# Performance work log

Measured on AMD Instinct MI355X. Metric: run time of the kernel, lower is better.

Reference implementation:

```python
import jax, jax.numpy as jnp
import numpy as np

DT = 0.01  # module-level constant in the original source
H = 64


def _lstm_cell(x_in, h, c, W_ih, W_hh, b_ih, b_hh):
    # torch nn.LSTM gate order: i, f, g, o
    gates = x_in @ W_ih.T + h @ W_hh.T + (b_ih + b_hh)
    i, f, g, o = jnp.split(gates, 4, axis=-1)
    i = jax.nn.sigmoid(i)
    f = jax.nn.sigmoid(f)
    g = jnp.tanh(g)
    o = jax.nn.sigmoid(o)
    c_new = f * c + i * g
    h_new = o * jnp.tanh(c_new)
    return h_new, c_new


def setup_inputs() -> dict:
    key = jax.random.key(0)
    ks = jax.random.split(key, 12)
    B, x_size, s_size = 4096, 8, 8
    in_size = x_size + s_size
    sc = 1.0 / np.sqrt(H)

    def rn(k, shape, scale=1.0):
        return (jax.random.normal(k, shape, dtype=jnp.float32) * scale)

    return {
        "x": rn(ks[0], (B, 1, x_size)),
        "s0": rn(ks[1], (B, s_size)),
        "W_ih0": rn(ks[2], (4 * H, in_size), sc),
        "W_hh0": rn(ks[3], (4 * H, H), sc),
        "b_ih0": rn(ks[4], (4 * H,), sc),
        "b_hh0": rn(ks[5], (4 * H,), sc),
        "W_ih1": rn(ks[6], (4 * H, H), sc),
        "W_hh1": rn(ks[7], (4 * H, H), sc),
        "b_ih1": rn(ks[8], (4 * H,), sc),
        "b_hh1": rn(ks[9], (4 * H,), sc),
        "fc_W": rn(ks[10], (s_size, H), sc),
        "fc_b": rn(ks[11], (s_size,), sc),
        "num_steps": 1001,  # floor(max_time/dt)+1 with max_time=10.0
    }


def reference(x, s0, W_ih0, W_hh0, b_ih0, b_hh0, W_ih1, W_hh1, b_ih1, b_hh1,
              fc_W, fc_b, num_steps):
    B = x.shape[0]
    xin = x[:, 0, :]  # forward only ever reads x[:, 0:1] -> [B, x_size]
    h0 = jnp.zeros((B, H), x.dtype)

    def step(carry, _):
        s, h_a, c_a, h_b, c_b = carry
        combined = jnp.concatenate([xin, s], axis=-1)  # [B, x_size + s_size]
        h_a, c_a = _lstm_cell(combined, h_a, c_a, W_ih0, W_hh0, b_ih0, b_hh0)
        h_b, c_b = _lstm_cell(h_a, h_b, c_b, W_ih1, W_hh1, b_ih1, b_hh1)
        step_out = h_b @ fc_W.T + fc_b            # [B, s_size]
        s_new = s + step_out * DT                  # Euler integration
        return (s_new, h_a, c_a, h_b, c_b), (s_new, step_out)

    init = (s0, h0, h0, h0, h0)
    _, (outs, res) = jax.lax.scan(step, init, None, length=num_steps)
    outputs = jnp.transpose(outs, (1, 0, 2))       # [B, num_steps, s_size]
    res_step = jnp.transpose(res, (1, 0, 2))       # [B, num_steps, s_size]
    cal_times = jnp.arange(num_steps, dtype=jnp.float32) * DT
    return outputs, cal_times, res_step
```

## Files before the change

kernel.cpp:

```cpp
#include <hip/hip_runtime.h>

#define DTC 0.01f
#define LAM  2.88539008178f
#define L2E  1.44269504089f

typedef __attribute__((ext_vector_type(8))) short short8;
typedef __attribute__((ext_vector_type(4))) float floatx4;

#if __has_builtin(__builtin_amdgcn_exp2f)
#define EXP2F(x) __builtin_amdgcn_exp2f(x)
#else
#define EXP2F(x) exp2f(x)
#endif
#if __has_builtin(__builtin_amdgcn_rcpf)
#define RCPF(x) __builtin_amdgcn_rcpf(x)
#else
#define RCPF(x) (1.0f / (x))
#endif

__device__ __forceinline__ unsigned short f2bf(float f) {
    unsigned u = __float_as_uint(f);
    u += 0x7FFFu + ((u >> 16) & 1u);
    return (unsigned short)(u >> 16);
}
__device__ __forceinline__ float rcp1p(float y) {
    return RCPF(1.0f + EXP2F(y));
}
__device__ __forceinline__ void wg_barrier() {
    asm volatile("s_waitcnt lgkmcnt(0)" ::: "memory");
    __builtin_amdgcn_s_barrier();
}

#define U1S 136

#define MFMA(a, b, c) __builtin_amdgcn_mfma_f32_16x16x32_bf16((a), (b), (c), 0, 0, 0)

__global__ __launch_bounds__(256, 1) void lstm_mfma(
    const float* __restrict__ x,    const float* __restrict__ s0,
    const float* __restrict__ W_ih0,const float* __restrict__ W_hh0,
    const float* __restrict__ b_ih0,const float* __restrict__ b_hh0,
    const float* __restrict__ W_ih1,const float* __restrict__ W_hh1,
    const float* __restrict__ b_ih1,const float* __restrict__ b_hh1,
    const float* __restrict__ fc_W, const float* __restrict__ fc_b,
    const int* __restrict__ nsp,    float* __restrict__ out, int B)
{
    __shared__ __align__(16) unsigned short U1[16 * U1S];

    const int ns   = nsp[0];
    const int tid  = threadIdx.x;
    const int lane = tid & 63;
    const int wave = tid >> 6;
    const int il   = lane & 15;
    const int quad = lane >> 4;
    const int bb   = blockIdx.x * 16;

    float* cal = out + (size_t)B * ns * 8;
    float* res = cal + ns;

    if (blockIdx.x == 0)
        for (int t = tid; t < ns; t += 256) cal[t] = t * DTC;

    for (int i = tid; i < 16 * U1S; i += 256) U1[i] = 0;

    short8 B0[4][2], B1[4][4], M2f[4][2], BF[2];
    floatx4 gs[4], bias1v[4];
    float gd[4];

    for (int j = 0; j < 4; ++j) {
        const float gam = (j == 2) ? LAM : -L2E;
        const int n = 64 * j + 16 * wave + il;
        float ws[8];
        #pragma unroll
        for (int p = 0; p < 8; ++p) ws[p] = W_ih0[n * 16 + 8 + p];

        #pragma unroll
        for (int kk = 0; kk < 2; ++kk) {
            short8 f;
            #pragma unroll
            for (int jj = 0; jj < 8; ++jj) {
                int k = 32 * kk + 8 * quad + jj;
                f[jj] = (short)f2bf(gam * W_hh0[n * 64 + k]);
            }
            B0[j][kk] = f;
        }
        #pragma unroll
        for (int kk = 0; kk < 4; ++kk) {
            short8 f;
            #pragma unroll
            for (int jj = 0; jj < 8; ++jj) {
                int k = 32 * kk + 8 * quad + jj;
                float w = (k < 64) ? W_ih1[n * 64 + k] : W_hh1[n * 64 + (k - 64)];
                f[jj] = (short)f2bf(gam * w);
            }
            B1[j][kk] = f;
        }
        #pragma unroll
        for (int kk = 0; kk < 2; ++kk) {
            short8 f;
            #pragma unroll
            for (int jj = 0; jj < 8; ++jj) {
                int k = 32 * kk + 8 * quad + jj;
                float acc = 0.0f;
                #pragma unroll
                for (int p = 0; p < 8; ++p) acc += ws[p] * fc_W[p * 64 + k];
                f[jj] = (short)f2bf(gam * DTC * acc);
            }
            M2f[j][kk] = f;
        }
        float accb = 0.0f;
        #pragma unroll
        for (int p = 0; p < 8; ++p) accb += ws[p] * fc_b[p];
        gd[j] = gam * DTC * accb;

        float bcol = b_ih0[n] + b_hh0[n];
        floatx4 gv;
        #pragma unroll
        for (int reg = 0; reg < 4; ++reg) {
            int m = 4 * quad + reg;
            float acc = bcol;
            #pragma unroll
            for (int k = 0; k < 8; ++k) acc += x[(bb + m) * 8 + k] * W_ih0[n * 16 + k];
            #pragma unroll
            for (int p = 0; p < 8; ++p) acc += ws[p] * s0[(bb + m) * 8 + p];
            gv[reg] = gam * acc - gd[j];
        }
        gs[j] = gv;
        float b1 = gam * (b_ih1[n] + b_hh1[n]);
        bias1v[j] = (floatx4){b1, b1, b1, b1};
    }
    #pragma unroll
    for (int kk = 0; kk < 2; ++kk) {
        short8 f;
        #pragma unroll
        for (int jj = 0; jj < 8; ++jj) {
            int k = 32 * kk + 8 * quad + jj;
            float w = (il < 8) ? fc_W[il * 64 + k] : 0.0f;
            f[jj] = (short)f2bf(w);
        }
        BF[kk] = f;
    }
    const float fcb = (il < 8) ? fc_b[il] : 0.0f;

    float cA[4] = {0, 0, 0, 0}, cB[4] = {0, 0, 0, 0};
    float s_reg[4];
    #pragma unroll
    for (int reg = 0; reg < 4; ++reg) {
        int m = 4 * quad + reg;
        s_reg[reg] = (il < 8) ? s0[(bb + m) * 8 + il] : 0.0f;
    }

    short8 a10 = {0, 0, 0, 0, 0, 0, 0, 0};
    short8 a11 = {0, 0, 0, 0, 0, 0, 0, 0};
    const int iidx = 16 * wave + il;
    wg_barrier();

    #pragma unroll 1
    for (int t = 0; t < ns; ++t) {
        short8 a12 = *(const short8*)&U1[il * U1S + 64 + 8 * quad];
        short8 a13 = *(const short8*)&U1[il * U1S + 96 + 8 * quad];

        floatx4 g0[4];
        #pragma unroll
        for (int j = 0; j < 4; ++j) {
            floatx4 z = {0.f, 0.f, 0.f, 0.f};
            z = MFMA(a10, B0[j][0], z);
            z = MFMA(a11, B0[j][1], z);
            g0[j] = z;
        }
        #pragma unroll
        for (int j = 0; j < 4; ++j) {
            floatx4 z = gs[j];
            z = MFMA(a12, M2f[j][0], z);
            z = MFMA(a13, M2f[j][1], z);
            #pragma unroll
            for (int reg = 0; reg < 4; ++reg) z[reg] += gd[j];
            gs[j] = z;
        }
        floatx4 p1[4];
        #pragma unroll
        for (int j = 0; j < 4; ++j) {
            floatx4 z = bias1v[j];
            z = MFMA(a12, B1[j][2], z);
            z = MFMA(a13, B1[j][3], z);
            p1[j] = z;
        }
        #pragma unroll
        for (int reg = 0; reg < 4; ++reg) {
            float iv = rcp1p(g0[0][reg] + gs[0][reg]);
            float fv = rcp1p(g0[1][reg] + gs[1][reg]);
            float gr = rcp1p(g0[2][reg] + gs[2][reg]);
            float gl = __builtin_fmaf(gr, -2.0f * LAM, LAM);
            float ov = rcp1p(g0[3][reg] + gs[3][reg]);
            float c  = __builtin_fmaf(fv, cA[reg], iv * gl);
            cA[reg]  = c;
            float r2 = rcp1p(c);
            float u  = ov * r2;
            float h  = __builtin_fmaf(-2.0f, u, ov);
            U1[(4 * quad + reg) * U1S + iidx] = f2bf(h);
        }
        wg_barrier();

        a10 = *(const short8*)&U1[il * U1S + 0  + 8 * quad];
        a11 = *(const short8*)&U1[il * U1S + 32 + 8 * quad];

        if (t && wave == 0) {
            floatx4 so = {fcb, fcb, fcb, fcb};
            so = MFMA(a12, BF[0], so);
            so = MFMA(a13, BF[1], so);
            #pragma unroll
            for (int reg = 0; reg < 4; ++reg) {
                s_reg[reg] += so[reg] * DTC;
                if (il < 8) {
                    int m = 4 * quad + reg;
                    size_t o = ((size_t)(bb + m) * ns + (t - 1)) * 8 + il;
                    out[o] = s_reg[reg];
                    res[o] = so[reg];
                }
            }
        }

        floatx4 g1[4];
        #pragma unroll
        for (int j = 0; j < 4; ++j) {
            floatx4 z = p1[j];
            z = MFMA(a10, B1[j][0], z);
            z = MFMA(a11, B1[j][1], z);
            g1[j] = z;
        }
        #pragma unroll
        for (int reg = 0; reg < 4; ++reg) {
            float iv = rcp1p(g1[0][reg]);
            float fv = rcp1p(g1[1][reg]);
            float gr = rcp1p(g1[2][reg]);
            float gl = __builtin_fmaf(gr, -2.0f * LAM, LAM);
            float ov = rcp1p(g1[3][reg]);
            float c  = __builtin_fmaf(fv, cB[reg], iv * gl);
            cB[reg]  = c;
            float r2 = rcp1p(c);
            float u  = ov * r2;
            float h  = __builtin_fmaf(-2.0f, u, ov);
            U1[(4 * quad + reg) * U1S + 64 + iidx] = f2bf(h);
        }
        wg_barrier();
    }

    if (wave == 0) {
        short8 a12 = *(const short8*)&U1[il * U1S + 64 + 8 * quad];
        short8 a13 = *(const short8*)&U1[il * U1S + 96 + 8 * quad];
        floatx4 so = {fcb, fcb, fcb, fcb};
        so = MFMA(a12, BF[0], so);
        so = MFMA(a13, BF[1], so);
        #pragma unroll
        for (int reg = 0; reg < 4; ++reg) {
            s_reg[reg] += so[reg] * DTC;
            if (il < 8) {
                int m = 4 * quad + reg;
                size_t o = ((size_t)(bb + m) * ns + (ns - 1)) * 8 + il;
                out[o] = s_reg[reg];
                res[o] = so[reg];
            }
        }
    }
}

extern "C" void kernel_launch(void* const* d_in, const int* in_sizes, int n_in,
                              void* d_out, int out_size, void* d_ws, size_t ws_size,
                              hipStream_t stream) {
    const float* x     = (const float*)d_in[0];
    const float* s0    = (const float*)d_in[1];
    const float* W_ih0 = (const float*)d_in[2];
    const float* W_hh0 = (const float*)d_in[3];
    const float* b_ih0 = (const float*)d_in[4];
    const float* b_hh0 = (const float*)d_in[5];
    const float* W_ih1 = (const float*)d_in[6];
    const float* W_hh1 = (const float*)d_in[7];
    const float* b_ih1 = (const float*)d_in[8];
    const float* b_hh1 = (const float*)d_in[9];
    const float* fc_W  = (const float*)d_in[10];
    const float* fc_b  = (const float*)d_in[11];
    const int*   nsp   = (const int*)d_in[12];
    (void)d_ws; (void)ws_size; (void)n_in; (void)out_size;
    int B = in_sizes[0] / 8;
    dim3 grid(B / 16), block(256);
    hipLaunchKernelGGL(lstm_mfma, grid, block, 0, stream,
        x, s0, W_ih0, W_hh0, b_ih0, b_hh0, W_ih1, W_hh1, b_ih1, b_hh1,
        fc_W, fc_b, nsp, (float*)d_out, B);
}
```

Measured before the change: 1.399 ms.

## Split gate computation across twice the waves with LDS exchange of preactivations

Doubles the workgroup from 4 to 8 waves so each wave computes two of the four gate blocks instead of all four. Gate preactivations are written to a new shared float buffer, and after a barrier each wave reads all four gates for its slice of elements to apply the cell update. This halves the MFMA and activation work per wave per step so more of the serial recurrence runs in parallel. In exchange it adds two extra workgroup barriers and LDS round trips per timestep on a latency-bound loop.

Result: slower. 1.501 ms (+7.2%).

```diff
diff --git a/kernel.cpp b/kernel.cpp
--- a/kernel.cpp
+++ b/kernel.cpp
@@ -32,10 +32,11 @@
 }
 
 #define U1S 136
+#define ES  68
 
 #define MFMA(a, b, c) __builtin_amdgcn_mfma_f32_16x16x32_bf16((a), (b), (c), 0, 0, 0)
 
-__global__ __launch_bounds__(256, 1) void lstm_mfma(
+__global__ __launch_bounds__(512, 1) void lstm_mfma(
     const float* __restrict__ x,    const float* __restrict__ s0,
     const float* __restrict__ W_ih0,const float* __restrict__ W_hh0,
     const float* __restrict__ b_ih0,const float* __restrict__ b_hh0,
@@ -45,6 +46,7 @@
     const int* __restrict__ nsp,    float* __restrict__ out, int B)
 {
     __shared__ __align__(16) unsigned short U1[16 * U1S];
+    __shared__ float E[4 * 16 * ES];
 
     const int ns   = nsp[0];
     const int tid  = threadIdx.x;
@@ -52,26 +54,30 @@
     const int wave = tid >> 6;
     const int il   = lane & 15;
     const int quad = lane >> 4;
+    const int g    = wave >> 1;
+    const int p    = wave & 1;
+    const int col  = 16 * g + il;
     const int bb   = blockIdx.x * 16;
 
     float* cal = out + (size_t)B * ns * 8;
     float* res = cal + ns;
 
     if (blockIdx.x == 0)
-        for (int t = tid; t < ns; t += 256) cal[t] = t * DTC;
-
-    for (int i = tid; i < 16 * U1S; i += 256) U1[i] = 0;
-
-    short8 B0[4][2], B1[4][4], M2f[4][2], BF[2];
-    floatx4 gs[4], bias1v[4];
-    float gd[4];
-
-    for (int j = 0; j < 4; ++j) {
+        for (int t = tid; t < ns; t += 512) cal[t] = t * DTC;
+
+    for (int i = tid; i < 16 * U1S; i += 512) U1[i] = 0;
+
+    short8 B0[2][2], B1[2][4], M2f[2][2], BF[2];
+    floatx4 gs[2];
+    float gd[2], b1s[2];
+
+    for (int jl = 0; jl < 2; ++jl) {
+        const int j = 2 * p + jl;
         const float gam = (j == 2) ? LAM : -L2E;
-        const int n = 64 * j + 16 * wave + il;
+        const int n = 64 * j + col;
         float ws[8];
         #pragma unroll
-        for (int p = 0; p < 8; ++p) ws[p] = W_ih0[n * 16 + 8 + p];
+        for (int pp = 0; pp < 8; ++pp) ws[pp] = W_ih0[n * 16 + 8 + pp];
 
         #pragma unroll
         for (int kk = 0; kk < 2; ++kk) {
@@ -81,7 +87,7 @@
                 int k = 32 * kk + 8 * quad + jj;
                 f[jj] = (short)f2bf(gam * W_hh0[n * 64 + k]);
             }
-            B0[j][kk] = f;
+            B0[jl][kk] = f;
         }
         #pragma unroll
         for (int kk = 0; kk < 4; ++kk) {
@@ -92,7 +98,7 @@
                 float w = (k < 64) ? W_ih1[n * 64 + k] : W_hh1[n * 64 + (k - 64)];
                 f[jj] = (short)f2bf(gam * w);
             }
-            B1[j][kk] = f;
+            B1[jl][kk] = f;
         }
         #pragma unroll
         for (int kk = 0; kk < 2; ++kk) {
@@ -102,15 +108,15 @@
                 int k = 32 * kk + 8 * quad + jj;
                 float acc = 0.0f;
                 #pragma unroll
-                for (int p = 0; p < 8; ++p) acc += ws[p] * fc_W[p * 64 + k];
+                for (int pp = 0; pp < 8; ++pp) acc += ws[pp] * fc_W[pp * 64 + k];
                 f[jj] = (short)f2bf(gam * DTC * acc);
             }
-            M2f[j][kk] = f;
+            M2f[jl][kk] = f;
         }
         float accb = 0.0f;
         #pragma unroll
-        for (int p = 0; p < 8; ++p) accb += ws[p] * fc_b[p];
-        gd[j] = gam * DTC * accb;
+        for (int pp = 0; pp < 8; ++pp) accb += ws[pp] * fc_b[pp];
+        gd[jl] = gam * DTC * accb;
 
         float bcol = b_ih0[n] + b_hh0[n];
         floatx4 gv;
@@ -121,12 +127,11 @@
             #pragma unroll
             for (int k = 0; k < 8; ++k) acc += x[(bb + m) * 8 + k] * W_ih0[n * 16 + k];
             #pragma unroll
-            for (int p = 0; p < 8; ++p) acc += ws[p] * s0[(bb + m) * 8 + p];
-            gv[reg] = gam * acc - gd[j];
-        }
-        gs[j] = gv;
-        float b1 = gam * (b_ih1[n] + b_hh1[n]);
-        bias1v[j] = (floatx4){b1, b1, b1, b1};
+            for (int pp = 0; pp < 8; ++pp) acc += ws[pp] * s0[(bb + m) * 8 + pp];
+            gv[reg] = gam * acc - gd[jl];
+        }
+        gs[jl] = gv;
+        b1s[jl] = gam * (b_ih1[n] + b_hh1[n]);
     }
     #pragma unroll
     for (int kk = 0; kk < 2; ++kk) {
@@ -141,67 +146,70 @@
     }
     const float fcb = (il < 8) ? fc_b[il] : 0.0f;
 
-    float cA[4] = {0, 0, 0, 0}, cB[4] = {0, 0, 0, 0};
+    float cA[2] = {0, 0}, cB[2] = {0, 0};
     float s_reg[4];
     #pragma unroll
-    for (int reg = 0; reg < 4; ++reg) {
-        int m = 4 * quad + reg;
-        s_reg[reg] = (il < 8) ? s0[(bb + m) * 8 + il] : 0.0f;
-    }
-
-    short8 a10 = {0, 0, 0, 0, 0, 0, 0, 0};
-    short8 a11 = {0, 0, 0, 0, 0, 0, 0, 0};
-    const int iidx = 16 * wave + il;
+    for (int reg = 0; reg < 4; ++reg)
+        s_reg[reg] = (il < 8) ? s0[(bb + 4 * quad + reg) * 8 + il] : 0.0f;
+
+    short8 a10 = {0,0,0,0,0,0,0,0};
+    short8 a11 = {0,0,0,0,0,0,0,0};
+    floatx4 p1[2];
+
+    const unsigned short* Ar = &U1[il * U1S + 8 * quad];
+    unsigned short* Hw = &U1[(8 * p + 2 * quad) * U1S + col];
+    float* Ew = &E[(32 * p + 4 * quad) * ES + col];
+    const float* Er = &E[(8 * p + 2 * quad) * ES + col];
+
     wg_barrier();
 
     #pragma unroll 1
     for (int t = 0; t < ns; ++t) {
-        short8 a12 = *(const short8*)&U1[il * U1S + 64 + 8 * quad];
-        short8 a13 = *(const short8*)&U1[il * U1S + 96 + 8 * quad];
-
-        floatx4 g0[4];
-        #pragma unroll
-        for (int j = 0; j < 4; ++j) {
-            floatx4 z = {0.f, 0.f, 0.f, 0.f};
-            z = MFMA(a10, B0[j][0], z);
-            z = MFMA(a11, B0[j][1], z);
-            g0[j] = z;
-        }
-        #pragma unroll
-        for (int j = 0; j < 4; ++j) {
-            floatx4 z = gs[j];
-            z = MFMA(a12, M2f[j][0], z);
-            z = MFMA(a13, M2f[j][1], z);
-            #pragma unroll
-            for (int reg = 0; reg < 4; ++reg) z[reg] += gd[j];
-            gs[j] = z;
-        }
-        floatx4 p1[4];
-        #pragma unroll
-        for (int j = 0; j < 4; ++j) {
-            floatx4 z = bias1v[j];
-            z = MFMA(a12, B1[j][2], z);
-            z = MFMA(a13, B1[j][3], z);
-            p1[j] = z;
-        }
-        #pragma unroll
-        for (int reg = 0; reg < 4; ++reg) {
-            float iv = rcp1p(g0[0][reg] + gs[0][reg]);
-            float fv = rcp1p(g0[1][reg] + gs[1][reg]);
-            float gr = rcp1p(g0[2][reg] + gs[2][reg]);
+        short8 a12 = *(const short8*)(Ar + 64);
+        short8 a13 = *(const short8*)(Ar + 96);
+
+        #pragma unroll
+        for (int jl = 0; jl < 2; ++jl) {
+            floatx4 z = gs[jl];
+            z = MFMA(a12, M2f[jl][0], z);
+            z = MFMA(a13, M2f[jl][1], z);
+            #pragma unroll
+            for (int r = 0; r < 4; ++r) z[r] += gd[jl];
+            gs[jl] = z;
+            floatx4 q = z;
+            q = MFMA(a10, B0[jl][0], q);
+            q = MFMA(a11, B0[jl][1], q);
+            #pragma unroll
+            for (int r = 0; r < 4; ++r)
+                Ew[jl * (16 * ES) + r * ES] = q[r];
+            floatx4 pz = {b1s[jl], b1s[jl], b1s[jl], b1s[jl]};
+            pz = MFMA(a13, B1[jl][3], pz);
+            pz = MFMA(a12, B1[jl][2], pz);
+            p1[jl] = pz;
+        }
+        wg_barrier();
+
+        #pragma unroll
+        for (int e = 0; e < 2; ++e) {
+            float pi = Er[e * ES + 0 * (16 * ES)];
+            float pf = Er[e * ES + 1 * (16 * ES)];
+            float pg = Er[e * ES + 2 * (16 * ES)];
+            float po = Er[e * ES + 3 * (16 * ES)];
+            float iv = rcp1p(pi);
+            float fv = rcp1p(pf);
+            float gr = rcp1p(pg);
+            float ov = rcp1p(po);
             float gl = __builtin_fmaf(gr, -2.0f * LAM, LAM);
-            float ov = rcp1p(g0[3][reg] + gs[3][reg]);
-            float c  = __builtin_fmaf(fv, cA[reg], iv * gl);
-            cA[reg]  = c;
+            float c  = __builtin_fmaf(fv, cA[e], iv * gl);
+            cA[e]    = c;
             float r2 = rcp1p(c);
-            float u  = ov * r2;
-            float h  = __builtin_fmaf(-2.0f, u, ov);
-            U1[(4 * quad + reg) * U1S + iidx] = f2bf(h);
+            float h  = __builtin_fmaf(-2.0f, ov * r2, ov);
+            Hw[e * U1S] = f2bf(h);
         }
         wg_barrier();
 
-        a10 = *(const short8*)&U1[il * U1S + 0  + 8 * quad];
-        a11 = *(const short8*)&U1[il * U1S + 32 + 8 * quad];
+        a10 = *(const short8*)(Ar + 0);
+        a11 = *(const short8*)(Ar + 32);
 
         if (t && wave == 0) {
             floatx4 so = {fcb, fcb, fcb, fcb};
@@ -211,42 +219,47 @@
             for (int reg = 0; reg < 4; ++reg) {
                 s_reg[reg] += so[reg] * DTC;
                 if (il < 8) {
-                    int m = 4 * quad + reg;
-                    size_t o = ((size_t)(bb + m) * ns + (t - 1)) * 8 + il;
+                    size_t o = ((size_t)(bb + 4 * quad + reg) * ns + (t - 1)) * 8 + il;
                     out[o] = s_reg[reg];
                     res[o] = so[reg];
                 }
             }
         }
 
-        floatx4 g1[4];
-        #pragma unroll
-        for (int j = 0; j < 4; ++j) {
-            floatx4 z = p1[j];
-            z = MFMA(a10, B1[j][0], z);
-            z = MFMA(a11, B1[j][1], z);
-            g1[j] = z;
-        }
-        #pragma unroll
-        for (int reg = 0; reg < 4; ++reg) {
-            float iv = rcp1p(g1[0][reg]);
-            float fv = rcp1p(g1[1][reg]);
-            float gr = rcp1p(g1[2][reg]);
+        #pragma unroll
+        for (int jl = 0; jl < 2; ++jl) {
+            floatx4 z = p1[jl];
+            z = MFMA(a10, B1[jl][0], z);
+            z = MFMA(a11, B1[jl][1], z);
+            #pragma unroll
+            for (int r = 0; r < 4; ++r)
+                Ew[jl * (16 * ES) + r * ES] = z[r];
+        }
+        wg_barrier();
+
+        #pragma unroll
+        for (int e = 0; e < 2; ++e) {
+            float pi = Er[e * ES + 0 * (16 * ES)];
+            float pf = Er[e * ES + 1 * (16 * ES)];
+            float pg = Er[e * ES + 2 * (16 * ES)];
+            float po = Er[e * ES + 3 * (16 * ES)];
+            float iv = rcp1p(pi);
+            float fv = rcp1p(pf);
+            float gr = rcp1p(pg);
+            float ov = rcp1p(po);
             float gl = __builtin_fmaf(gr, -2.0f * LAM, LAM);
-            float ov = rcp1p(g1[3][reg]);
-            float c  = __builtin_fmaf(fv, cB[reg], iv * gl);
-            cB[reg]  = c;
+            float c  = __builtin_fmaf(fv, cB[e], iv * gl);
+            cB[e]    = c;
             float r2 = rcp1p(c);
-            float u  = ov * r2;
-            float h  = __builtin_fmaf(-2.0f, u, ov);
-            U1[(4 * quad + reg) * U1S + 64 + iidx] = f2bf(h);
+            float h  = __builtin_fmaf(-2.0f, ov * r2, ov);
+            Hw[e * U1S + 64] = f2bf(h);
         }
         wg_barrier();
     }
 
     if (wave == 0) {
-        short8 a12 = *(const short8*)&U1[il * U1S + 64 + 8 * quad];
-        short8 a13 = *(const short8*)&U1[il * U1S + 96 + 8 * quad];
+        short8 a12 = *(const short8*)(Ar + 64);
+        short8 a13 = *(const short8*)(Ar + 96);
         floatx4 so = {fcb, fcb, fcb, fcb};
         so = MFMA(a12, BF[0], so);
         so = MFMA(a13, BF[1], so);
@@ -254,8 +267,7 @@
         for (int reg = 0; reg < 4; ++reg) {
             s_reg[reg] += so[reg] * DTC;
             if (il < 8) {
-                int m = 4 * quad + reg;
-                size_t o = ((size_t)(bb + m) * ns + (ns - 1)) * 8 + il;
+                size_t o = ((size_t)(bb + 4 * quad + reg) * ns + (ns - 1)) * 8 + il;
                 out[o] = s_reg[reg];
                 res[o] = so[reg];
             }
@@ -281,7 +293,7 @@
     const int*   nsp   = (const int*)d_in[12];
     (void)d_ws; (void)ws_size; (void)n_in; (void)out_size;
     int B = in_sizes[0] / 8;
-    dim3 grid(B / 16), block(256);
+    dim3 grid(B / 16), block(512);
     hipLaunchKernelGGL(lstm_mfma, grid, block, 0, stream,
         x, s0, W_ih0, W_hh0, b_ih0, b_hh0, W_ih1, W_hh1, b_ih1, b_hh1,
         fc_W, fc_b, nsp, (float*)d_out, B);
```

## Halve batch rows per block, duplicate rows and split gate math via permlane swap

Applied to the files above, without the earlier changes.

Each block now handles 8 batch rows instead of 16, and the grid doubles to 512 blocks with launch bounds allowing two blocks per CU. The 16-row MFMA tile holds each row twice, and permlane32_swap lets each lane take two distinct elements, so every lane runs half the transcendental gate math. This cuts per-step serial latency on the recurrence critical path. In exchange, half of every MFMA is redundant and two blocks must share a CU's registers. The layer-0 gate accumulation is also reordered so the state MFMAs chain directly into the gate sums.

New measurement: 1.561 ms. +11.6%, slower.

```diff
diff --git a/kernel.cpp b/kernel.cpp
--- a/kernel.cpp
+++ b/kernel.cpp
@@ -30,12 +30,24 @@
     asm volatile("s_waitcnt lgkmcnt(0)" ::: "memory");
     __builtin_amdgcn_s_barrier();
 }
+__device__ __forceinline__ float lane_merge(float lo, float hi) {
+#if __has_builtin(__builtin_amdgcn_permlane32_swap)
+    typedef __attribute__((ext_vector_type(2))) unsigned int uint2v;
+    uint2v r = __builtin_amdgcn_permlane32_swap(__float_as_uint(lo), __float_as_uint(hi),
+                                                false, false);
+    return __uint_as_float(r[0]);
+#else
+    unsigned a = __float_as_uint(lo), b = __float_as_uint(hi);
+    asm volatile("v_permlane32_swap_b32 %0, %1" : "+v"(a), "+v"(b));
+    return __uint_as_float(a);
+#endif
+}
 
 #define U1S 136
 
 #define MFMA(a, b, c) __builtin_amdgcn_mfma_f32_16x16x32_bf16((a), (b), (c), 0, 0, 0)
 
-__global__ __launch_bounds__(256, 1) void lstm_mfma(
+__global__ __launch_bounds__(256, 2) void lstm_mfma(
     const float* __restrict__ x,    const float* __restrict__ s0,
     const float* __restrict__ W_ih0,const float* __restrict__ W_hh0,
     const float* __restrict__ b_ih0,const float* __restrict__ b_hh0,
@@ -52,7 +64,7 @@
     const int wave = tid >> 6;
     const int il   = lane & 15;
     const int quad = lane >> 4;
-    const int bb   = blockIdx.x * 16;
+    const int bb   = blockIdx.x * 8;
 
     float* cal = out + (size_t)B * ns * 8;
     float* res = cal + ns;
@@ -63,8 +75,8 @@
     for (int i = tid; i < 16 * U1S; i += 256) U1[i] = 0;
 
     short8 B0[4][2], B1[4][4], M2f[4][2], BF[2];
-    floatx4 gs[4], bias1v[4];
-    float gd[4];
+    floatx4 gs[4];
+    float gd[4], b1s[4];
 
     for (int j = 0; j < 4; ++j) {
         const float gam = (j == 2) ? LAM : -L2E;
@@ -116,17 +128,17 @@
         floatx4 gv;
         #pragma unroll
         for (int reg = 0; reg < 4; ++reg) {
-            int m = 4 * quad + reg;
+            int m  = 4 * quad + reg;
+            int mr = bb + (m & 7);
             float acc = bcol;
             #pragma unroll
-            for (int k = 0; k < 8; ++k) acc += x[(bb + m) * 8 + k] * W_ih0[n * 16 + k];
-            #pragma unroll
-            for (int p = 0; p < 8; ++p) acc += ws[p] * s0[(bb + m) * 8 + p];
+            for (int k = 0; k < 8; ++k) acc += x[mr * 8 + k] * W_ih0[n * 16 + k];
+            #pragma unroll
+            for (int p = 0; p < 8; ++p) acc += ws[p] * s0[mr * 8 + p];
             gv[reg] = gam * acc - gd[j];
         }
         gs[j] = gv;
-        float b1 = gam * (b_ih1[n] + b_hh1[n]);
-        bias1v[j] = (floatx4){b1, b1, b1, b1};
+        b1s[j] = gam * (b_ih1[n] + b_hh1[n]);
     }
     #pragma unroll
     for (int kk = 0; kk < 2; ++kk) {
@@ -141,67 +153,70 @@
     }
     const float fcb = (il < 8) ? fc_b[il] : 0.0f;
 
-    float cA[4] = {0, 0, 0, 0}, cB[4] = {0, 0, 0, 0};
+    const int mbase = 4 * ((lane & 31) >> 4) + ((lane >> 5) << 1);
+    const int iidx  = 16 * wave + il;
+    float cA[2] = {0, 0}, cB[2] = {0, 0};
     float s_reg[4];
     #pragma unroll
     for (int reg = 0; reg < 4; ++reg) {
         int m = 4 * quad + reg;
-        s_reg[reg] = (il < 8) ? s0[(bb + m) * 8 + il] : 0.0f;
-    }
-
-    short8 a10 = {0, 0, 0, 0, 0, 0, 0, 0};
-    short8 a11 = {0, 0, 0, 0, 0, 0, 0, 0};
-    const int iidx = 16 * wave + il;
+        s_reg[reg] = (il < 8 && m < 8) ? s0[(bb + m) * 8 + il] : 0.0f;
+    }
+
+    short8 a10 = {0,0,0,0,0,0,0,0};
+    short8 a11 = {0,0,0,0,0,0,0,0};
+
+    const unsigned short* Ar = &U1[il * U1S + 8 * quad];
+    unsigned short* Hw = &U1[mbase * U1S + iidx];
+
     wg_barrier();
 
     #pragma unroll 1
     for (int t = 0; t < ns; ++t) {
-        short8 a12 = *(const short8*)&U1[il * U1S + 64 + 8 * quad];
-        short8 a13 = *(const short8*)&U1[il * U1S + 96 + 8 * quad];
-
-        floatx4 g0[4];
-        #pragma unroll
-        for (int j = 0; j < 4; ++j) {
-            floatx4 z = {0.f, 0.f, 0.f, 0.f};
-            z = MFMA(a10, B0[j][0], z);
-            z = MFMA(a11, B0[j][1], z);
-            g0[j] = z;
-        }
+        short8 a12 = *(const short8*)(Ar + 64);
+        short8 a13 = *(const short8*)(Ar + 96);
+
+        floatx4 q0[4], p1[4];
         #pragma unroll
         for (int j = 0; j < 4; ++j) {
             floatx4 z = gs[j];
             z = MFMA(a12, M2f[j][0], z);
             z = MFMA(a13, M2f[j][1], z);
             #pragma unroll
-            for (int reg = 0; reg < 4; ++reg) z[reg] += gd[j];
+            for (int r = 0; r < 4; ++r) z[r] += gd[j];
             gs[j] = z;
-        }
-        floatx4 p1[4];
+            floatx4 q = z;
+            q = MFMA(a10, B0[j][0], q);
+            q = MFMA(a11, B0[j][1], q);
+            q0[j] = q;
+            floatx4 pz = {b1s[j], b1s[j], b1s[j], b1s[j]};
+            pz = MFMA(a13, B1[j][3], pz);
+            pz = MFMA(a12, B1[j][2], pz);
+            p1[j] = pz;
+        }
+        float P[2][4];
         #pragma unroll
         for (int j = 0; j < 4; ++j) {
-            floatx4 z = bias1v[j];
-            z = MFMA(a12, B1[j][2], z);
-            z = MFMA(a13, B1[j][3], z);
-            p1[j] = z;
-        }
-        #pragma unroll
-        for (int reg = 0; reg < 4; ++reg) {
-            float iv = rcp1p(g0[0][reg] + gs[0][reg]);
-            float fv = rcp1p(g0[1][reg] + gs[1][reg]);
-            float gr = rcp1p(g0[2][reg] + gs[2][reg]);
+            P[0][j] = lane_merge(q0[j][0], q0[j][2]);
+            P[1][j] = lane_merge(q0[j][1], q0[j][3]);
+        }
+        #pragma unroll
+        for (int e = 0; e < 2; ++e) {
+            float iv = rcp1p(P[e][0]);
+            float fv = rcp1p(P[e][1]);
+            float gr = rcp1p(P[e][2]);
+            float ov = rcp1p(P[e][3]);
             float gl = __builtin_fmaf(gr, -2.0f * LAM, LAM);
-            float ov = rcp1p(g0[3][reg] + gs[3][reg]);
-            float c  = __builtin_fmaf(fv, cA[reg], iv * gl);
-            cA[reg]  = c;
+            float c  = __builtin_fmaf(fv, cA[e], iv * gl);
+            cA[e]    = c;
             float r2 = rcp1p(c);
-            float u  = ov * r2;
-            float h  = __builtin_fmaf(-2.0f, u, ov);
-            U1[(4 * quad + reg) * U1S + iidx] = f2bf(h);
+            float h  = __builtin_fmaf(-2.0f, ov * r2, ov);
+            Hw[e * U1S] = f2bf(h);
         }
         wg_barrier();
 
-        a10 = *(const short8*)&U1[il * U1S + 0  + 8 * quad];
-        a11 = *(const short8*)&U1[il * U1S + 32 + 8 * quad];
+        a10 = *(const short8*)(Ar + 0);
+        a11 = *(const short8*)(Ar + 32);
 
         if (t && wave == 0) {
             floatx4 so = {fcb, fcb, fcb, fcb};
@@ -210,52 +225,55 @@
             #pragma unroll
             for (int reg = 0; reg < 4; ++reg) {
                 s_reg[reg] += so[reg] * DTC;
-                if (il < 8) {
-                    int m = 4 * quad + reg;
-                    size_t o = ((size_t)(bb + m) * ns + (t - 1)) * 8 + il;
+                if (quad < 2 && il < 8) {
+                    size_t o = ((size_t)(bb + 4 * quad + reg) * ns + (t - 1)) * 8 + il;
                     out[o] = s_reg[reg];
                     res[o] = so[reg];
                 }
             }
         }
 
-        floatx4 g1[4];
+        floatx4 q1[4];
         #pragma unroll
         for (int j = 0; j < 4; ++j) {
             floatx4 z = p1[j];
             z = MFMA(a10, B1[j][0], z);
             z = MFMA(a11, B1[j][1], z);
-            g1[j] = z;
-        }
-        #pragma unroll
-        for (int reg = 0; reg < 4; ++reg) {
-            float iv = rcp1p(g1[0][reg]);
-            float fv = rcp1p(g1[1][reg]);
-            float gr = rcp1p(g1[2][reg]);
+            q1[j] = z;
+        }
+        float Q[2][4];
+        #pragma unroll
+        for (int j = 0; j < 4; ++j) {
+            Q[0][j] = lane_merge(q1[j][0], q1[j][2]);
+            Q[1][j] = lane_merge(q1[j][1], q1[j][3]);
+        }
+        #pragma unroll
+        for (int e = 0; e < 2; ++e) {
+            float iv = rcp1p(Q[e][0]);
+            float fv = rcp1p(Q[e][1]);
+            float gr = rcp1p(Q[e][2]);
+            float ov = rcp1p(Q[e][3]);
             float gl = __builtin_fmaf(gr, -2.0f * LAM, LAM);
-            float ov = rcp1p(g1[3][reg]);
-            float c  = __builtin_fmaf(fv, cB[reg], iv * gl);
-            cB[reg]  = c;
+            float c  = __builtin_fmaf(fv, cB[e], iv * gl);
+            cB[e]    = c;
             float r2 = rcp1p(c);
-            float u  = ov * r2;
-            float h  = __builtin_fmaf(-2.0f, u, ov);
-            U1[(4 * quad + reg) * U1S + 64 + iidx] = f2bf(h);
+            float h  = __builtin_fmaf(-2.0f, ov * r2, ov);
+            Hw[e * U1S + 64] = f2bf(h);
         }
         wg_barrier();
     }
 
     if (wave == 0) {
-        short8 a12 = *(const short8*)&U1[il * U1S + 64 + 8 * quad];
-        short8 a13 = *(const short8*)&U1[il * U1S + 96 + 8 * quad];
+        short8 a12 = *(const short8*)(Ar + 64);
+        short8 a13 = *(const short8*)(Ar + 96);
         floatx4 so = {fcb, fcb, fcb, fcb};
         so = MFMA(a12, BF[0], so);
         so = MFMA(a13, BF[1], so);
         #pragma unroll
         for (int reg = 0; reg < 4; ++reg) {
             s_reg[reg] += so[reg] * DTC;
-            if (il < 8) {
-                int m = 4 * quad + reg;
-                size_t o = ((size_t)(bb + m) * ns + (ns - 1)) * 8 + il;
+            if (quad < 2 && il < 8) {
+                size_t o = ((size_t)(bb + 4 * quad + reg) * ns + (ns - 1)) * 8 + il;
                 out[o] = s_reg[reg];
                 res[o] = so[reg];
             }
@@ -281,7 +299,7 @@
     const int*   nsp   = (const int*)d_in[12];
     (void)d_ws; (void)ws_size; (void)n_in; (void)out_size;
     int B = in_sizes[0] / 8;
-    dim3 grid(B / 16), block(256);
+    dim3 grid(B / 8), block(256);
     hipLaunchKernelGGL(lstm_mfma, grid, block, 0, stream,
         x, s0, W_ih0, W_hh0, b_ih0, b_hh0, W_ih1, W_hh1, b_ih1, b_hh1,
         fc_W, fc_b, nsp, (float*)d_out, B);
```
